# Kernel optimization log

Measured on AMD Instinct MI355X. Metric: run time of the kernel, lower is better.

Reference implementation:

```python
import jax, jax.numpy as jnp
import numpy as np

N, K, E = 100000, 256, 3200000
IN_C, H1, H2 = 5, 16, 32


def _glorot(key, shape):
    fan = shape[0]
    return jax.random.normal(key, shape, jnp.float32) / np.float32(np.sqrt(fan))


def setup_inputs() -> dict:
    key = jax.random.key(0)
    ks = jax.random.split(key, 14)
    x = jax.random.normal(ks[0], (N, IN_C), jnp.float32)
    edge_index = jax.random.randint(ks[1], (2, E), 0, N, dtype=jnp.int64)
    edge_attr = jax.random.uniform(ks[2], (E,), jnp.float32)
    pos = jax.random.uniform(ks[3], (N, K), jnp.float32)  # soft cluster assignment s_c
    return {
        "x": x, "edge_index": edge_index, "edge_attr": edge_attr, "pos": pos,
        # SplineConv1 (kernel_size=1 -> single kernel weight + root + bias)
        "W1": _glorot(ks[4], (IN_C, H1)), "root1": _glorot(ks[5], (IN_C, H1)),
        "b1": jnp.zeros((H1,), jnp.float32),
        # SplineConv2
        "W2": _glorot(ks[6], (H1, H2)), "root2": _glorot(ks[7], (H1, H2)),
        "b2": jnp.zeros((H2,), jnp.float32),
        # MLP head
        "lw1": _glorot(ks[8], (H2, 8)), "lb1": jnp.zeros((8,), jnp.float32),
        "lw2": _glorot(ks[9], (8, 2)), "lb2": jnp.zeros((2,), jnp.float32),
    }


def _leaky(v):
    return jnp.where(v > 0, v, 0.1 * v)


def reference(x, edge_index, edge_attr, pos, W1, root1, b1, W2, root2, b2, lw1, lb1, lw2, lb2):
    n = x.shape[0]
    src, dst = edge_index[0], edge_index[1]  # source_to_target flow

    # --- SplineConv(5,16,dim=1,kernel_size=1): mean_j (x_j @ W) + x @ root + b ---
    msg = x[src] @ W1                                      # [E,16]
    agg = jax.ops.segment_sum(msg, dst, num_segments=n)    # [N,16]
    deg = jax.ops.segment_sum(jnp.ones((msg.shape[0],), x.dtype), dst, num_segments=n)
    h = agg / jnp.maximum(deg, 1.0)[:, None] + x @ root1 + b1
    h = _leaky(jax.nn.relu(h))                             # relu then LeakyReLU(0.1)

    # --- pooling: x' = s_c^T h ; adj = s_c^T A s_c (A sparse with edge_attr values) ---
    xp = pos.T @ h                                          # [K,16]
    A_sc = jax.ops.segment_sum(edge_attr[:, None] * pos[dst], src, num_segments=n)  # spmm: [N,K]
    adj = pos.T @ A_sc                                      # [K,K]

    # --- nonzero/coalesce -> edge list of adj; SplineConv(16,32) on pooled graph ---
    # kernel_size=1 => edge values irrelevant; only the nonzero pattern (connectivity) matters.
    mask = (adj != 0).astype(x.dtype)                       # [K,K], row=src, col=dst
    xw = xp @ W2                                            # [K,32]
    deg2 = mask.sum(axis=0)                                 # in-degree per target
    agg2 = (mask.T @ xw) / jnp.maximum(deg2, 1.0)[:, None]
    h2 = agg2 + xp @ root2 + b2
    h2 = _leaky(jax.nn.relu(h2))                            # [K,32]

    # --- global mean pool (single graph) + MLP head, return x[0] ---
    g = h2.mean(axis=0)                                     # [32]
    out = _leaky(g @ lw1 + lb1) @ lw2 + lb2                 # [2]
    return out
```

## Files before the change

### kernel.cpp

```cpp
#include <hip/hip_runtime.h>

#define INC 5
#define H1C 16
#define H2C 32
#define KCL 256

#define NBINS 40
#define BINSZ 2500
#define MAXCHUNK 12

#define PB_SHIFT 9
#define PB_SZ 512
#define PB_NBMAX 256
#define PB_C 18432
#define PB_M 6144
#define PB_ETPB 6
#define PB_S 2
#define PB_GMAX 9216
#define PB_GETG 9

#define POOL_NB 768
#define PCH 256

typedef __attribute__((address_space(1))) const unsigned gls_src;
typedef __attribute__((address_space(3))) unsigned gls_dst;

__global__ void k_setup(const float* __restrict__ x, float* __restrict__ x8,
                        const unsigned int* __restrict__ ei, int* __restrict__ flag,
                        unsigned* __restrict__ gcur, int N, int NB) {
    int n = blockIdx.x * blockDim.x + threadIdx.x;
    if (n < N) {
        const float* xr = x + (size_t)n * INC;
        float4* o = (float4*)(x8 + (size_t)n * 8);
        o[0] = make_float4(xr[0], xr[1], xr[2], xr[3]);
        o[1] = make_float4(xr[4], 0.0f, 0.0f, 0.0f);
    }
    if (blockIdx.x == 0) {
        if (threadIdx.x < (unsigned)NB) gcur[threadIdx.x] = (unsigned)threadIdx.x * PB_C;
        if (threadIdx.x == 0) {
            int is64 = 1;
            for (int i = 1; i < 32; i += 2)
                if (ei[i] != 0u) is64 = 0;
            *flag = is64;
        }
    }
}

__global__ void k_detect(const unsigned int* __restrict__ ei, int* __restrict__ flag) {
    if (blockIdx.x == 0 && threadIdx.x == 0) {
        int is64 = 1;
        for (int i = 1; i < 32; i += 2)
            if (ei[i] != 0u) is64 = 0;
        *flag = is64;
    }
}

__global__ __launch_bounds__(1024) void k_part(const unsigned int* __restrict__ ei,
                                               const int* __restrict__ flag,
                                               unsigned* __restrict__ gcur,
                                               unsigned* __restrict__ bucket,
                                               int E, int NB) {
    __shared__ int hist[PB_NBMAX];
    __shared__ int lbase[PB_NBMAX];
    __shared__ unsigned gbase[PB_NBMAX];
    __shared__ unsigned sorted[PB_M];
    __shared__ unsigned char sbin[PB_M];

    const int tid = threadIdx.x;
    const int e0 = blockIdx.x * PB_M;
    int m = E - e0; if (m > PB_M) m = PB_M;

    for (int i = tid; i < PB_NBMAX; i += 1024) hist[i] = 0;
    __syncthreads();

    const int is64 = *flag;
    unsigned ee[PB_ETPB]; int eb[PB_ETPB]; int er[PB_ETPB];

#pragma unroll
    for (int ii = 0; ii < PB_ETPB; ii++) {
        const int off = tid + ii * 1024;
        eb[ii] = -1; ee[ii] = 0u; er[ii] = 0;
        if (off < m) {
            const int e = e0 + off;
            unsigned d, s;
            if (is64) { d = ei[2 * ((size_t)E + (size_t)e)]; s = ei[2 * (size_t)e]; }
            else      { d = ei[(size_t)E + (size_t)e];       s = ei[(size_t)e]; }
            const int b = (int)(d >> PB_SHIFT);
            eb[ii] = b;
            ee[ii] = (s << PB_SHIFT) | (d & (PB_SZ - 1));
            er[ii] = atomicAdd(&hist[b], 1);
        }
    }
    __syncthreads();

    if (tid < 64) {
        const int base = tid * 4;
        int vals[4]; int s = 0;
#pragma unroll
        for (int k = 0; k < 4; k++) { vals[k] = hist[base + k]; s += vals[k]; }
        int t = s;
#pragma unroll
        for (int off = 1; off < 64; off <<= 1) {
            int y = __shfl_up(t, off);
            if (tid >= off) t += y;
        }
        int ex = t - s;
#pragma unroll
        for (int k = 0; k < 4; k++) { lbase[base + k] = ex; ex += vals[k]; }
    }
    if (tid >= 64 && tid < 64 + NB) {
        const int b = tid - 64;
        gbase[b] = atomicAdd(&gcur[b], (unsigned)hist[b]);
    }
    __syncthreads();

#pragma unroll
    for (int ii = 0; ii < PB_ETPB; ii++) {
        if (eb[ii] >= 0) {
            const int j = lbase[eb[ii]] + er[ii];
            sorted[j] = ee[ii];
            sbin[j] = (unsigned char)eb[ii];
        }
    }
    __syncthreads();

    for (int j = tid; j < m; j += 1024) {
        const int b = (int)sbin[j];
        const unsigned g = gbase[b] + (unsigned)(j - lbase[b]);
        if (g < (unsigned)(b + 1) * PB_C) bucket[g] = sorted[j];
    }
}

__global__ __launch_bounds__(1024) void k_gather(const unsigned* __restrict__ bucket,
                                                 const unsigned* __restrict__ gcur,
                                                 const float* __restrict__ x8,
                                                 float* __restrict__ part,
                                                 int N, int NB) {
    __shared__ unsigned sorted[PB_GMAX];
    __shared__ int hist[PB_SZ];
    __shared__ int lbase[PB_SZ];
    __shared__ float stage[PB_SZ * 6];

    const int b = blockIdx.x / PB_S;
    const int sub = blockIdx.x % PB_S;
    const int tid = threadIdx.x;
    const int lo = b << PB_SHIFT;
    int hi = lo + PB_SZ; if (hi > N) hi = N;
    const int nloc = hi - lo;

    int cnt = (int)(gcur[b] - (unsigned)b * PB_C);
    if (cnt > PB_C) cnt = PB_C;
    const int i0 = (cnt * sub) / PB_S;
    const int i1 = (cnt * (sub + 1)) / PB_S;
    const int m = i1 - i0;
    const unsigned* bk = bucket + (size_t)b * PB_C + i0;

    for (int i = tid; i < PB_SZ; i += 1024) hist[i] = 0;
    __syncthreads();

    unsigned ee[PB_GETG]; int edl[PB_GETG]; int er[PB_GETG];
#pragma unroll
    for (int ii = 0; ii < PB_GETG; ii++) {
        const int off = tid + ii * 1024;
        edl[ii] = -1; ee[ii] = 0u; er[ii] = 0;
        if (off < m) {
            const unsigned e = bk[off];
            const int dl = (int)(e & (PB_SZ - 1));
            edl[ii] = dl;
            ee[ii] = e;
            er[ii] = atomicAdd(&hist[dl], 1);
        }
    }
    __syncthreads();

    if (tid < 64) {
        const int base = tid * 8;
        int vals[8]; int s = 0;
#pragma unroll
        for (int k = 0; k < 8; k++) { vals[k] = hist[base + k]; s += vals[k]; }
        int t = s;
#pragma unroll
        for (int off = 1; off < 64; off <<= 1) {
            int y = __shfl_up(t, off);
            if (tid >= off) t += y;
        }
        int ex = t - s;
#pragma unroll
        for (int k = 0; k < 8; k++) { lbase[base + k] = ex; ex += vals[k]; }
    }
    __syncthreads();

#pragma unroll
    for (int ii = 0; ii < PB_GETG; ii++)
        if (edl[ii] >= 0) sorted[lbase[edl[ii]] + er[ii]] = ee[ii];
    __syncthreads();

    const int node = tid & (PB_SZ - 1);
    const int half = tid >> PB_SHIFT;
    const int start = lbase[node];
    const int len = hist[node];
    const int js = start + (half ? (len >> 1) : 0);
    const int je = start + (half ? len : (len >> 1));
    float a0 = 0.f, a1 = 0.f, a2 = 0.f, a3 = 0.f, a4 = 0.f;
    for (int j = js; j < je; j++) {
        const unsigned s = sorted[j] >> PB_SHIFT;
        const float4 xr4 = *(const float4*)(x8 + (size_t)s * 8);
        const float xr5 = x8[(size_t)s * 8 + 4];
        a0 += xr4.x; a1 += xr4.y; a2 += xr4.z; a3 += xr4.w; a4 += xr5;
    }
    if (half) {
        float* st = stage + node * 6;
        st[0] = a0; st[1] = a1; st[2] = a2; st[3] = a3; st[4] = a4;
    }
    __syncthreads();
    if (!half && node < nloc) {
        const float* st = stage + node * 6;
        float* o = part + (size_t)sub * ((size_t)N * 6) + (size_t)(lo + node) * 6;
        o[0] = a0 + st[0];
        o[1] = a1 + st[1];
        o[2] = a2 + st[2];
        o[3] = a3 + st[3];
        o[4] = a4 + st[4];
        o[5] = (float)len;
    }
}

__global__ __launch_bounds__(1024) void k_edge_bin(const unsigned int* __restrict__ ei,
                                                   const float* __restrict__ x,
                                                   const int* __restrict__ flag,
                                                   float* __restrict__ part,
                                                   int E, int nchunk, int N) {
    __shared__ float acc[BINSZ * 6];
    const int bin = blockIdx.x % NBINS;
    const int chunk = blockIdx.x / NBINS;
    const int lo = bin * BINSZ;
    const int hi = (lo + BINSZ < N) ? (lo + BINSZ) : N;
    const int nloc = hi - lo;
    for (int i = threadIdx.x; i < nloc * 6; i += 1024) acc[i] = 0.0f;
    __syncthreads();

    const int is64 = *flag;
    const long long ce = ((long long)E + nchunk - 1) / nchunk;
    const long long e0 = (long long)chunk * ce;
    long long e1 = e0 + ce;
    if (e1 > E) e1 = E;

    for (long long e = e0 + threadIdx.x; e < e1; e += 1024) {
        const int d = is64 ? (int)ei[2 * ((size_t)E + (size_t)e)] : (int)ei[(size_t)E + (size_t)e];
        if (d >= lo && d < hi) {
            const int s = is64 ? (int)ei[2 * (size_t)e] : (int)ei[(size_t)e];
            const float* xr = x + (size_t)s * INC;
            float* a = acc + (d - lo) * 6;
            atomicAdd(a + 0, xr[0]);
            atomicAdd(a + 1, xr[1]);
            atomicAdd(a + 2, xr[2]);
            atomicAdd(a + 3, xr[3]);
            atomicAdd(a + 4, xr[4]);
            atomicAdd(a + 5, 1.0f);
        }
    }
    __syncthreads();
    float* o = part + (size_t)chunk * ((size_t)N * 6) + (size_t)lo * 6;
    for (int i = threadIdx.x; i < nloc * 6; i += 1024) o[i] = acc[i];
}

__global__ void k_node2(const float* __restrict__ x, const float* __restrict__ part,
                        const float* __restrict__ W1, const float* __restrict__ root1,
                        const float* __restrict__ b1, float* __restrict__ h,
                        int N, int nchunk) {
    int n = blockIdx.x * blockDim.x + threadIdx.x;
    if (n >= N) return;
    float s[6] = {0.f, 0.f, 0.f, 0.f, 0.f, 0.f};
    for (int c = 0; c < nchunk; c++) {
        const float* p = part + (size_t)c * ((size_t)N * 6) + (size_t)n * 6;
#pragma unroll
        for (int j = 0; j < 6; j++) s[j] += p[j];
    }
    const float inv = 1.0f / fmaxf(s[5], 1.0f);
    float xs[INC], xv[INC];
#pragma unroll
    for (int c = 0; c < INC; c++) {
        xs[c] = s[c] * inv;
        xv[c] = x[(size_t)n * INC + c];
    }
    float hv[H1C];
#pragma unroll
    for (int j = 0; j < H1C; j++) {
        float v = b1[j];
#pragma unroll
        for (int c = 0; c < INC; c++)
            v = fmaf(xs[c], W1[c * H1C + j], fmaf(xv[c], root1[c * H1C + j], v));
        hv[j] = fmaxf(v, 0.0f);
    }
    float4* hp = (float4*)(h + (size_t)n * H1C);
#pragma unroll
    for (int q = 0; q < 4; q++)
        hp[q] = make_float4(hv[4 * q], hv[4 * q + 1], hv[4 * q + 2], hv[4 * q + 3]);
}

__global__ __launch_bounds__(256) void k_pool(const float* __restrict__ pos,
                                              const float* __restrict__ h,
                                              const float* __restrict__ part,
                                              const float* __restrict__ x8,
                                              const float* __restrict__ W1,
                                              const float* __restrict__ root1,
                                              const float* __restrict__ b1,
                                              float* __restrict__ xp_part, int N, int nb) {
    __shared__ float hbuf[PCH * H1C];
    __shared__ float sred[2][32][64];
    const int tid = threadIdx.x;
    const int lane = tid & 63;
    const int w = tid >> 6;
    const int chunk = (N + nb - 1) / nb;
    const int n0 = blockIdx.x * chunk;
    const int n1 = min(n0 + chunk, N);
    const int cnt = (n1 > n0) ? (n1 - n0) : 0;

    if (part) {
        if (tid < cnt) {
            const int n = n0 + tid;
            const float* pa = part + (size_t)n * 6;
            const float* pb = part + (size_t)N * 6 + (size_t)n * 6;
            float s[6];
#pragma unroll
            for (int j = 0; j < 6; j++) s[j] = pa[j] + pb[j];
            const float inv = 1.0f / fmaxf(s[5], 1.0f);
            float xs[INC], xv[INC];
#pragma unroll
            for (int c = 0; c < INC; c++) {
                xs[c] = s[c] * inv;
                xv[c] = x8[(size_t)n * 8 + c];
            }
#pragma unroll
            for (int j = 0; j < H1C; j++) {
                float v = b1[j];
#pragma unroll
                for (int c = 0; c < INC; c++)
                    v = fmaf(xs[c], W1[c * H1C + j], fmaf(xv[c], root1[c * H1C + j], v));
                hbuf[tid * H1C + j] = fmaxf(v, 0.0f);
            }
        }
    } else {
        const size_t maxh = (size_t)N * H1C - 4;
        for (int ii = w; ii * 256 < cnt * H1C; ii += 4) {
            size_t fi = (size_t)n0 * H1C + (size_t)ii * 256 + (size_t)lane * 4;
            if (fi > maxh) fi = maxh;
            __builtin_amdgcn_global_load_lds((gls_src*)(h + fi),
                                             (gls_dst*)&hbuf[ii * 256], 16, 0, 0);
        }
    }
    __syncthreads();

    float acc[4][H1C];
#pragma unroll
    for (int c = 0; c < 4; c++)
#pragma unroll
        for (int d = 0; d < H1C; d++) acc[c][d] = 0.0f;

    const float4* pos4 = (const float4*)pos;
    const float4 z4 = make_float4(0.f, 0.f, 0.f, 0.f);

#define LDP(dst, i)                                                        \
    {                                                                      \
        const int _i = (i);                                                \
        if (_i < cnt) dst = pos4[((size_t)n0 + _i) * 64 + lane];           \
    }
#define CMP(i, p)                                                          \
    {                                                                      \
        const int _i = (i);                                                \
        if (_i < cnt) {                                                    \
            const float4 h0 = *(const float4*)&hbuf[_i * H1C + 0];         \
            const float4 h1 = *(const float4*)&hbuf[_i * H1C + 4];         \
            const float4 h2 = *(const float4*)&hbuf[_i * H1C + 8];         \
            const float4 h3 = *(const float4*)&hbuf[_i * H1C + 12];        \
            const float pk[4] = {p.x, p.y, p.z, p.w};                      \
            const float hv[H1C] = {h0.x, h0.y, h0.z, h0.w,                 \
                                   h1.x, h1.y, h1.z, h1.w,                 \
                                   h2.x, h2.y, h2.z, h2.w,                 \
                                   h3.x, h3.y, h3.z, h3.w};                \
            _Pragma("unroll")                                              \
            for (int c = 0; c < 4; c++)                                    \
                _Pragma("unroll")                                          \
                for (int d = 0; d < H1C; d++)                              \
                    acc[c][d] = fmaf(pk[c], hv[d], acc[c][d]);             \
        }                                                                  \
    }

    float4 A0 = z4, A1 = z4, A2 = z4, A3 = z4;
    float4 B0 = z4, B1 = z4, B2 = z4, B3 = z4;
    float4 C0 = z4, C1 = z4, C2 = z4, C3 = z4;
    float4 D0 = z4, D1 = z4, D2 = z4, D3 = z4;
    LDP(A0, w + 0)  LDP(A1, w + 4)  LDP(A2, w + 8)  LDP(A3, w + 12)
    LDP(B0, w + 16) LDP(B1, w + 20) LDP(B2, w + 24) LDP(B3, w + 28)
    LDP(C0, w + 32) LDP(C1, w + 36) LDP(C2, w + 40) LDP(C3, w + 44)
    LDP(D0, w + 48) LDP(D1, w + 52) LDP(D2, w + 56) LDP(D3, w + 60)
    for (int i = w; i < cnt; i += 64) {
        CMP(i + 0, A0)  CMP(i + 4, A1)  CMP(i + 8, A2)  CMP(i + 12, A3)
        LDP(A0, i + 64) LDP(A1, i + 68) LDP(A2, i + 72) LDP(A3, i + 76)
        CMP(i + 16, B0) CMP(i + 20, B1) CMP(i + 24, B2) CMP(i + 28, B3)
        LDP(B0, i + 80) LDP(B1, i + 84) LDP(B2, i + 88) LDP(B3, i + 92)
        CMP(i + 32, C0) CMP(i + 36, C1) CMP(i + 40, C2) CMP(i + 44, C3)
        LDP(C0, i + 96) LDP(C1, i + 100) LDP(C2, i + 104) LDP(C3, i + 108)
        CMP(i + 48, D0) CMP(i + 52, D1) CMP(i + 56, D2) CMP(i + 60, D3)
        LDP(D0, i + 112) LDP(D1, i + 116) LDP(D2, i + 120) LDP(D3, i + 124)
    }
#undef LDP
#undef CMP

    __syncthreads();
#pragma unroll
    for (int ch = 0; ch < 2; ch++) {
        if (w == 1 || w == 3) {
            float* sl = &sred[(w - 1) >> 1][0][0] + lane;
#pragma unroll
            for (int v = 0; v < 32; v++) sl[v * 64] = acc[ch * 2 + (v >> 4)][v & 15];
        }
        __syncthreads();
        if (w == 0 || w == 2) {
            const float* sl = &sred[w >> 1][0][0] + lane;
#pragma unroll
            for (int v = 0; v < 32; v++) acc[ch * 2 + (v >> 4)][v & 15] += sl[v * 64];
        }
        __syncthreads();
        if (w == 2) {
            float* sl = &sred[0][0][0] + lane;
#pragma unroll
            for (int v = 0; v < 32; v++) sl[v * 64] = acc[ch * 2 + (v >> 4)][v & 15];
        }
        __syncthreads();
        if (w == 0) {
            const float* sl = &sred[0][0][0] + lane;
#pragma unroll
            for (int v = 0; v < 32; v++) acc[ch * 2 + (v >> 4)][v & 15] += sl[v * 64];
        }
        __syncthreads();
    }
    if (w == 0) {
        float* o = xp_part + (size_t)blockIdx.x * (KCL * H1C);
#pragma unroll
        for (int c = 0; c < 4; c++) {
            float* oc = o + (4 * lane + c) * H1C;
            *(float4*)(oc + 0)  = make_float4(acc[c][0],  acc[c][1],  acc[c][2],  acc[c][3]);
            *(float4*)(oc + 4)  = make_float4(acc[c][4],  acc[c][5],  acc[c][6],  acc[c][7]);
            *(float4*)(oc + 8)  = make_float4(acc[c][8],  acc[c][9],  acc[c][10], acc[c][11]);
            *(float4*)(oc + 12) = make_float4(acc[c][12], acc[c][13], acc[c][14], acc[c][15]);
        }
    }
}

__global__ __launch_bounds__(1024) void k_xpred(const float* __restrict__ xp_part,
                                                float* __restrict__ xp, int nb) {
    __shared__ float r[1024];
    const int li = threadIdx.x & 63;
    const int sub = threadIdx.x >> 6;
    const int i = blockIdx.x * 64 + li;
    float s = 0.0f;
    for (int b = sub; b < nb; b += 16) s += xp_part[(size_t)b * (KCL * H1C) + i];
    r[threadIdx.x] = s;
    __syncthreads();
    if (threadIdx.x < 512) r[threadIdx.x] += r[threadIdx.x + 512];
    __syncthreads();
    if (threadIdx.x < 256) r[threadIdx.x] += r[threadIdx.x + 256];
    __syncthreads();
    if (threadIdx.x < 128) r[threadIdx.x] += r[threadIdx.x + 128];
    __syncthreads();
    if (threadIdx.x < 64) xp[i] = r[threadIdx.x] + r[threadIdx.x + 64];
}

__global__ __launch_bounds__(256) void k_tail(const float* __restrict__ xp,
                                              const float* __restrict__ W2,
                                              const float* __restrict__ root2,
                                              const float* __restrict__ b2,
                                              const float* __restrict__ lw1,
                                              const float* __restrict__ lb1,
                                              const float* __restrict__ lw2,
                                              const float* __restrict__ lb2,
                                              float* __restrict__ out) {
    __shared__ float red[4][H2C];
    __shared__ float bcast[H2C];
    const int t = threadIdx.x;
    const int wv = t >> 6;
    const int lane = t & 63;

    float row[H1C];
#pragma unroll
    for (int c = 0; c < H1C; c++) row[c] = xp[t * H1C + c];

    float v1[H2C];
#pragma unroll
    for (int j = 0; j < H2C; j++) {
        float v = 0.0f;
#pragma unroll
        for (int c = 0; c < H1C; c++) v = fmaf(row[c], W2[c * H2C + j], v);
        v1[j] = v;
    }
#pragma unroll
    for (int off = 1; off < 64; off <<= 1) {
#pragma unroll
        for (int j = 0; j < H2C; j++) v1[j] += __shfl_xor(v1[j], off);
    }
    if (lane == 0) {
#pragma unroll
        for (int j = 0; j < H2C; j++) red[wv][j] = v1[j];
    }
    __syncthreads();
    if (t < H2C) bcast[t] = red[0][t] + red[1][t] + red[2][t] + red[3][t];
    __syncthreads();

    float v2[H2C];
#pragma unroll
    for (int j = 0; j < H2C; j++) {
        float v = bcast[j] * (1.0f / KCL) + b2[j];
#pragma unroll
        for (int c = 0; c < H1C; c++) v = fmaf(row[c], root2[c * H2C + j], v);
        v2[j] = fmaxf(v, 0.0f);
    }
#pragma unroll
    for (int off = 1; off < 64; off <<= 1) {
#pragma unroll
        for (int j = 0; j < H2C; j++) v2[j] += __shfl_xor(v2[j], off);
    }
    if (lane == 0) {
#pragma unroll
        for (int j = 0; j < H2C; j++) red[wv][j] = v2[j];
    }
    __syncthreads();

    if (t == 0) {
        float g[H2C];
#pragma unroll
        for (int j = 0; j < H2C; j++)
            g[j] = (red[0][j] + red[1][j] + red[2][j] + red[3][j]) * (1.0f / KCL);
        float u[8];
#pragma unroll
        for (int a = 0; a < 8; a++) {
            float v = lb1[a];
#pragma unroll
            for (int j = 0; j < H2C; j++) v = fmaf(g[j], lw1[j * 8 + a], v);
            u[a] = v > 0.0f ? v : 0.1f * v;
        }
#pragma unroll
        for (int o = 0; o < 2; o++) {
            float v = lb2[o];
#pragma unroll
            for (int a = 0; a < 8; a++) v = fmaf(u[a], lw2[a * 2 + o], v);
            out[o] = v;
        }
    }
}

extern "C" void kernel_launch(void* const* d_in, const int* in_sizes, int n_in,
                              void* d_out, int out_size, void* d_ws, size_t ws_size,
                              hipStream_t stream) {
    const float* x         = (const float*)d_in[0];
    const unsigned int* ei = (const unsigned int*)d_in[1];
    const float* pos   = (const float*)d_in[3];
    const float* W1    = (const float*)d_in[4];
    const float* root1 = (const float*)d_in[5];
    const float* b1    = (const float*)d_in[6];
    const float* W2    = (const float*)d_in[7];
    const float* root2 = (const float*)d_in[8];
    const float* b2    = (const float*)d_in[9];
    const float* lw1   = (const float*)d_in[10];
    const float* lb1   = (const float*)d_in[11];
    const float* lw2   = (const float*)d_in[12];
    const float* lb2   = (const float*)d_in[13];
    float* out = (float*)d_out;

    const int N = in_sizes[0] / INC;
    const int E = in_sizes[1] / 2;
    const int NB = (N + PB_SZ - 1) >> PB_SHIFT;

    float* ws    = (float*)d_ws;
    float* xp    = ws;
    int*   flag  = (int*)(xp + KCL * H1C);
    float* h     = (float*)(flag + 16);
    float* regio = h + (size_t)N * H1C;

    const size_t pref_floats = (size_t)(KCL * H1C) + 16 + (size_t)N * H1C;
    const size_t region_floats = ws_size / 4 > pref_floats ? ws_size / 4 - pref_floats : 0;
    const size_t slab_floats = (size_t)POOL_NB * (KCL * H1C);
    const size_t buck_floats = (size_t)NB * PB_C + 256;
    const size_t fast_floats = (size_t)PB_S * N * 6 + (size_t)N * 8 +
                               (buck_floats > slab_floats ? buck_floats : slab_floats);

    if (region_floats >= fast_floats && N <= 131072 && NB <= PB_NBMAX) {
        float* part      = regio;
        float* x8        = part + (size_t)PB_S * N * 6;
        unsigned* bucket = (unsigned*)(x8 + (size_t)N * 8);
        unsigned* gcur   = bucket + (size_t)NB * PB_C;
        const int P = (E + PB_M - 1) / PB_M;

        k_setup<<<(N + 255) / 256, 256, 0, stream>>>(x, x8, ei, flag, gcur, N, NB);
        k_part<<<P, 1024, 0, stream>>>(ei, flag, gcur, bucket, E, NB);
        k_gather<<<NB * PB_S, 1024, 0, stream>>>(bucket, gcur, x8, part, N, NB);

        float* xp_part = (float*)bucket;
        k_pool<<<POOL_NB, 256, 0, stream>>>(pos, nullptr, part, x8, W1, root1, b1,
                                            xp_part, N, POOL_NB);
        k_xpred<<<64, 1024, 0, stream>>>(xp_part, xp, POOL_NB);
    } else {
        size_t avail = region_floats > slab_floats ? region_floats - slab_floats : 0;
        int nchunk = (int)(avail / ((size_t)N * 6));
        if (nchunk > MAXCHUNK) nchunk = MAXCHUNK;
        if (nchunk < 1) nchunk = 1;
        float* part = regio;
        float* xp_part = part + (size_t)nchunk * N * 6;
        k_detect<<<1, 64, 0, stream>>>(ei, flag);
        k_edge_bin<<<NBINS * nchunk, 1024, 0, stream>>>(ei, x, flag, part, E, nchunk, N);
        k_node2<<<(N + 255) / 256, 256, 0, stream>>>(x, part, W1, root1, b1, h, N, nchunk);
        k_pool<<<POOL_NB, 256, 0, stream>>>(pos, h, nullptr, nullptr, W1, root1, b1,
                                            xp_part, N, POOL_NB);
        k_xpred<<<64, 1024, 0, stream>>>(xp_part, xp, POOL_NB);
    }
    k_tail<<<1, 256, 0, stream>>>(xp, W2, root2, b2, lw1, lb1, lw2, lb2, out);
}
```

Baseline: 108.8 us.

## Fuse setup/partition/gather and xp-reduce/tail into cooperative grid-synced kernels

Replaces the setup, partition and gather launches with one cooperative kernel that uses grid-wide syncs between phases and grid-strides over the work items. It also merges the xp slab reduction and the tail MLP into a second cooperative kernel. The aim is to remove kernel launch gaps and dependency bubbles between the small stages. In exchange, work is squeezed into a fixed 256-block grid with grid barriers, which may reduce occupancy and latency hiding in the partition and gather phases.

```diff
diff --git a/kernel.cpp b/kernel.cpp
--- a/kernel.cpp
+++ b/kernel.cpp
@@ -1,4 +1,7 @@
 #include <hip/hip_runtime.h>
+#include <hip/hip_cooperative_groups.h>
+
+namespace cg = cooperative_groups;
 
 #define INC 5
 #define H1C 16
@@ -22,8 +25,311 @@
 #define POOL_NB 768
 #define PCH 256
 
+#define MEGA_NB 256
+
 typedef __attribute__((address_space(1))) const unsigned gls_src;
 typedef __attribute__((address_space(3))) unsigned gls_dst;
+
+struct PartL {
+    unsigned sorted[PB_M];
+    unsigned char sbin[PB_M];
+    int hist[PB_NBMAX];
+    int lbase[PB_NBMAX];
+    unsigned gbase[PB_NBMAX];
+};
+struct GathL {
+    unsigned sorted[PB_GMAX];
+    int hist[PB_SZ];
+    int lbase[PB_SZ];
+    float stage[PB_SZ * 6];
+};
+union MegaL { PartL p; GathL g; };
+
+__global__ __launch_bounds__(1024) void k_mega1(const float* __restrict__ x,
+                                                const unsigned* __restrict__ ei,
+                                                unsigned* __restrict__ gcur,
+                                                unsigned* __restrict__ bucket,
+                                                float* __restrict__ x8,
+                                                float* __restrict__ part,
+                                                int N, int E, int NB, int P) {
+    __shared__ MegaL L;
+    cg::grid_group gg = cg::this_grid();
+    const int tid = threadIdx.x;
+
+    int is64 = 1;
+#pragma unroll
+    for (int i = 1; i < 32; i += 2)
+        if (ei[i] != 0u) is64 = 0;
+
+    {
+        const int n = blockIdx.x * 1024 + tid;
+        if (n < N) {
+            const float* xr = x + (size_t)n * INC;
+            float4* o = (float4*)(x8 + (size_t)n * 8);
+            o[0] = make_float4(xr[0], xr[1], xr[2], xr[3]);
+            o[1] = make_float4(xr[4], 0.0f, 0.0f, 0.0f);
+        }
+        if (n < NB) gcur[n] = (unsigned)n * PB_C;
+    }
+    gg.sync();
+
+    for (int vb = blockIdx.x; vb < P; vb += gridDim.x) {
+        const int e0 = vb * PB_M;
+        int m = E - e0; if (m > PB_M) m = PB_M;
+
+        for (int i = tid; i < PB_NBMAX; i += 1024) L.p.hist[i] = 0;
+        __syncthreads();
+
+        unsigned ee[PB_ETPB]; int eb[PB_ETPB]; int er[PB_ETPB];
+#pragma unroll
+        for (int ii = 0; ii < PB_ETPB; ii++) {
+            const int off = tid + ii * 1024;
+            eb[ii] = -1; ee[ii] = 0u; er[ii] = 0;
+            if (off < m) {
+                const int e = e0 + off;
+                unsigned d, s;
+                if (is64) { d = ei[2 * ((size_t)E + (size_t)e)]; s = ei[2 * (size_t)e]; }
+                else      { d = ei[(size_t)E + (size_t)e];       s = ei[(size_t)e]; }
+                const int b = (int)(d >> PB_SHIFT);
+                eb[ii] = b;
+                ee[ii] = (s << PB_SHIFT) | (d & (PB_SZ - 1));
+                er[ii] = atomicAdd(&L.p.hist[b], 1);
+            }
+        }
+        __syncthreads();
+
+        if (tid < 64) {
+            const int base = tid * 4;
+            int vals[4]; int s = 0;
+#pragma unroll
+            for (int k = 0; k < 4; k++) { vals[k] = L.p.hist[base + k]; s += vals[k]; }
+            int t = s;
+#pragma unroll
+            for (int off = 1; off < 64; off <<= 1) {
+                int y = __shfl_up(t, off);
+                if (tid >= off) t += y;
+            }
+            int ex = t - s;
+#pragma unroll
+            for (int k = 0; k < 4; k++) { L.p.lbase[base + k] = ex; ex += vals[k]; }
+        }
+        if (tid >= 64 && tid < 64 + NB) {
+            const int b = tid - 64;
+            L.p.gbase[b] = atomicAdd(&gcur[b], (unsigned)L.p.hist[b]);
+        }
+        __syncthreads();
+
+#pragma unroll
+        for (int ii = 0; ii < PB_ETPB; ii++) {
+            if (eb[ii] >= 0) {
+                const int j = L.p.lbase[eb[ii]] + er[ii];
+                L.p.sorted[j] = ee[ii];
+                L.p.sbin[j] = (unsigned char)eb[ii];
+            }
+        }
+        __syncthreads();
+
+        for (int j = tid; j < m; j += 1024) {
+            const int b = (int)L.p.sbin[j];
+            const unsigned g = L.p.gbase[b] + (unsigned)(j - L.p.lbase[b]);
+            if (g < (unsigned)(b + 1) * PB_C) bucket[g] = L.p.sorted[j];
+        }
+        __syncthreads();
+    }
+    gg.sync();
+
+    for (int vb = blockIdx.x; vb < NB * PB_S; vb += gridDim.x) {
+        const int b = vb / PB_S;
+        const int sub = vb % PB_S;
+        const int lo = b << PB_SHIFT;
+        int hi = lo + PB_SZ; if (hi > N) hi = N;
+        const int nloc = hi - lo;
+
+        int cnt = (int)(gcur[b] - (unsigned)b * PB_C);
+        if (cnt > PB_C) cnt = PB_C;
+        const int i0 = (cnt * sub) / PB_S;
+        const int i1 = (cnt * (sub + 1)) / PB_S;
+        const int m = i1 - i0;
+        const unsigned* bk = bucket + (size_t)b * PB_C + i0;
+
+        for (int i = tid; i < PB_SZ; i += 1024) L.g.hist[i] = 0;
+        __syncthreads();
+
+        unsigned ee[PB_GETG]; int edl[PB_GETG]; int er[PB_GETG];
+#pragma unroll
+        for (int ii = 0; ii < PB_GETG; ii++) {
+            const int off = tid + ii * 1024;
+            edl[ii] = -1; ee[ii] = 0u; er[ii] = 0;
+            if (off < m) {
+                const unsigned e = bk[off];
+                const int dl = (int)(e & (PB_SZ - 1));
+                edl[ii] = dl;
+                ee[ii] = e;
+                er[ii] = atomicAdd(&L.g.hist[dl], 1);
+            }
+        }
+        __syncthreads();
+
+        if (tid < 64) {
+            const int base = tid * 8;
+            int vals[8]; int s = 0;
+#pragma unroll
+            for (int k = 0; k < 8; k++) { vals[k] = L.g.hist[base + k]; s += vals[k]; }
+            int t = s;
+#pragma unroll
+            for (int off = 1; off < 64; off <<= 1) {
+                int y = __shfl_up(t, off);
+                if (tid >= off) t += y;
+            }
+            int ex = t - s;
+#pragma unroll
+            for (int k = 0; k < 8; k++) { L.g.lbase[base + k] = ex; ex += vals[k]; }
+        }
+        __syncthreads();
+
+#pragma unroll
+        for (int ii = 0; ii < PB_GETG; ii++)
+            if (edl[ii] >= 0) L.g.sorted[L.g.lbase[edl[ii]] + er[ii]] = ee[ii];
+        __syncthreads();
+
+        const int node = tid & (PB_SZ - 1);
+        const int half = tid >> PB_SHIFT;
+        const int start = L.g.lbase[node];
+        const int len = L.g.hist[node];
+        const int js = start + (half ? (len >> 1) : 0);
+        const int je = start + (half ? len : (len >> 1));
+        float a0 = 0.f, a1 = 0.f, a2 = 0.f, a3 = 0.f, a4 = 0.f;
+        for (int j = js; j < je; j++) {
+            const unsigned s = L.g.sorted[j] >> PB_SHIFT;
+            const float4 xr4 = *(const float4*)(x8 + (size_t)s * 8);
+            const float xr5 = x8[(size_t)s * 8 + 4];
+            a0 += xr4.x; a1 += xr4.y; a2 += xr4.z; a3 += xr4.w; a4 += xr5;
+        }
+        if (half) {
+            float* st = L.g.stage + node * 6;
+            st[0] = a0; st[1] = a1; st[2] = a2; st[3] = a3; st[4] = a4;
+        }
+        __syncthreads();
+        if (!half && node < nloc) {
+            const float* st = L.g.stage + node * 6;
+            float* o = part + (size_t)sub * ((size_t)N * 6) + (size_t)(lo + node) * 6;
+            o[0] = a0 + st[0];
+            o[1] = a1 + st[1];
+            o[2] = a2 + st[2];
+            o[3] = a3 + st[3];
+            o[4] = a4 + st[4];
+            o[5] = (float)len;
+        }
+        __syncthreads();
+    }
+}
+
+__global__ __launch_bounds__(256) void k_mega2(const float* __restrict__ xp_part,
+                                               float* __restrict__ xp,
+                                               const float* __restrict__ W2,
+                                               const float* __restrict__ root2,
+                                               const float* __restrict__ b2,
+                                               const float* __restrict__ lw1,
+                                               const float* __restrict__ lb1,
+                                               const float* __restrict__ lw2,
+                                               const float* __restrict__ lb2,
+                                               float* __restrict__ out, int nb) {
+    cg::grid_group gg = cg::this_grid();
+    __shared__ float r[256];
+    __shared__ float red[4][H2C];
+    __shared__ float bcast[H2C];
+    const int tid = threadIdx.x;
+
+    {
+        const int li = tid & 15;
+        const int sub = tid >> 4;
+        const int i = blockIdx.x * 16 + li;
+        float s = 0.0f;
+        for (int b = sub; b < nb; b += 16) s += xp_part[(size_t)b * (KCL * H1C) + i];
+        r[tid] = s;
+        __syncthreads();
+        if (tid < 128) r[tid] += r[tid + 128];
+        __syncthreads();
+        if (tid < 64) r[tid] += r[tid + 64];
+        __syncthreads();
+        if (tid < 32) r[tid] += r[tid + 32];
+        __syncthreads();
+        if (tid < 16) xp[blockIdx.x * 16 + tid] = r[tid] + r[tid + 16];
+    }
+    gg.sync();
+
+    if (blockIdx.x == 0) {
+        const int t = tid;
+        const int wv = t >> 6;
+        const int lane = t & 63;
+
+        float row[H1C];
+#pragma unroll
+        for (int c = 0; c < H1C; c++) row[c] = xp[t * H1C + c];
+
+        float v1[H2C];
+#pragma unroll
+        for (int j = 0; j < H2C; j++) {
+            float v = 0.0f;
+#pragma unroll
+            for (int c = 0; c < H1C; c++) v = fmaf(row[c], W2[c * H2C + j], v);
+            v1[j] = v;
+        }
+#pragma unroll
+        for (int off = 1; off < 64; off <<= 1) {
+#pragma unroll
+            for (int j = 0; j < H2C; j++) v1[j] += __shfl_xor(v1[j], off);
+        }
+        if (lane == 0) {
+#pragma unroll
+            for (int j = 0; j < H2C; j++) red[wv][j] = v1[j];
+        }
+        __syncthreads();
+        if (t < H2C) bcast[t] = red[0][t] + red[1][t] + red[2][t] + red[3][t];
+        __syncthreads();
+
+        float v2[H2C];
+#pragma unroll
+        for (int j = 0; j < H2C; j++) {
+            float v = bcast[j] * (1.0f / KCL) + b2[j];
+#pragma unroll
+            for (int c = 0; c < H1C; c++) v = fmaf(row[c], root2[c * H2C + j], v);
+            v2[j] = fmaxf(v, 0.0f);
+        }
+#pragma unroll
+        for (int off = 1; off < 64; off <<= 1) {
+#pragma unroll
+            for (int j = 0; j < H2C; j++) v2[j] += __shfl_xor(v2[j], off);
+        }
+        if (lane == 0) {
+#pragma unroll
+            for (int j = 0; j < H2C; j++) red[wv][j] = v2[j];
+        }
+        __syncthreads();
+
+        if (t == 0) {
+            float g[H2C];
+#pragma unroll
+            for (int j = 0; j < H2C; j++)
+                g[j] = (red[0][j] + red[1][j] + red[2][j] + red[3][j]) * (1.0f / KCL);
+            float u[8];
+#pragma unroll
+            for (int a = 0; a < 8; a++) {
+                float v = lb1[a];
+#pragma unroll
+                for (int j = 0; j < H2C; j++) v = fmaf(g[j] , lw1[j * 8 + a], v);
+                u[a] = v > 0.0f ? v : 0.1f * v;
+            }
+#pragma unroll
+            for (int o = 0; o < 2; o++) {
+                float v = lb2[o];
+#pragma unroll
+                for (int a = 0; a < 8; a++) v = fmaf(u[a], lw2[a * 2 + o], v);
+                out[o] = v;
+            }
+        }
+    }
+}
 
 __global__ void k_setup(const float* __restrict__ x, float* __restrict__ x8,
                         const unsigned int* __restrict__ ei, int* __restrict__ flag,
@@ -567,9 +873,9 @@
     const float* lb2   = (const float*)d_in[13];
     float* out = (float*)d_out;
 
-    const int N = in_sizes[0] / INC;
-    const int E = in_sizes[1] / 2;
-    const int NB = (N + PB_SZ - 1) >> PB_SHIFT;
+    int N = in_sizes[0] / INC;
+    int E = in_sizes[1] / 2;
+    int NB = (N + PB_SZ - 1) >> PB_SHIFT;
 
     float* ws    = (float*)d_ws;
     float* xp    = ws;
@@ -584,21 +890,46 @@
     const size_t fast_floats = (size_t)PB_S * N * 6 + (size_t)N * 8 +
                                (buck_floats > slab_floats ? buck_floats : slab_floats);
 
+    int coop = 0;
+    int dev = 0;
+    hipGetDevice(&dev);
+    hipDeviceGetAttribute(&coop, hipDeviceAttributeCooperativeLaunch, dev);
+
     if (region_floats >= fast_floats && N <= 131072 && NB <= PB_NBMAX) {
         float* part      = regio;
         float* x8        = part + (size_t)PB_S * N * 6;
         unsigned* bucket = (unsigned*)(x8 + (size_t)N * 8);
         unsigned* gcur   = bucket + (size_t)NB * PB_C;
-        const int P = (E + PB_M - 1) / PB_M;
-
-        k_setup<<<(N + 255) / 256, 256, 0, stream>>>(x, x8, ei, flag, gcur, N, NB);
-        k_part<<<P, 1024, 0, stream>>>(ei, flag, gcur, bucket, E, NB);
-        k_gather<<<NB * PB_S, 1024, 0, stream>>>(bucket, gcur, x8, part, N, NB);
-
+        int P = (E + PB_M - 1) / PB_M;
         float* xp_part = (float*)bucket;
-        k_pool<<<POOL_NB, 256, 0, stream>>>(pos, nullptr, part, x8, W1, root1, b1,
-                                            xp_part, N, POOL_NB);
-        k_xpred<<<64, 1024, 0, stream>>>(xp_part, xp, POOL_NB);
+        int nb_pool = POOL_NB;
+
+        if (coop) {
+            {
+                void* a1[] = {(void*)&x, (void*)&ei, (void*)&gcur, (void*)&bucket,
+                              (void*)&x8, (void*)&part, (void*)&N, (void*)&E,
+                              (void*)&NB, (void*)&P};
+                hipLaunchCooperativeKernel((const void*)k_mega1, dim3(MEGA_NB),
+                                           dim3(1024), a1, 0, stream);
+            }
+            k_pool<<<POOL_NB, 256, 0, stream>>>(pos, nullptr, part, x8, W1, root1, b1,
+                                                xp_part, N, POOL_NB);
+            {
+                void* a2[] = {(void*)&xp_part, (void*)&xp, (void*)&W2, (void*)&root2,
+                              (void*)&b2, (void*)&lw1, (void*)&lb1, (void*)&lw2,
+                              (void*)&lb2, (void*)&out, (void*)&nb_pool};
+                hipLaunchCooperativeKernel((const void*)k_mega2, dim3(256),
+                                           dim3(256), a2, 0, stream);
+            }
+        } else {
+            k_setup<<<(N + 255) / 256, 256, 0, stream>>>(x, x8, ei, flag, gcur, N, NB);
+            k_part<<<P, 1024, 0, stream>>>(ei, flag, gcur, bucket, E, NB);
+            k_gather<<<NB * PB_S, 1024, 0, stream>>>(bucket, gcur, x8, part, N, NB);
+            k_pool<<<POOL_NB, 256, 0, stream>>>(pos, nullptr, part, x8, W1, root1, b1,
+                                                xp_part, N, POOL_NB);
+            k_xpred<<<64, 1024, 0, stream>>>(xp_part, xp, POOL_NB);
+            k_tail<<<1, 256, 0, stream>>>(xp, W2, root2, b2, lw1, lb1, lw2, lb2, out);
+        }
     } else {
         size_t avail = region_floats > slab_floats ? region_floats - slab_floats : 0;
         int nchunk = (int)(avail / ((size_t)N * 6));
@@ -612,6 +943,6 @@
         k_pool<<<POOL_NB, 256, 0, stream>>>(pos, h, nullptr, nullptr, W1, root1, b1,
                                             xp_part, N, POOL_NB);
         k_xpred<<<64, 1024, 0, stream>>>(xp_part, xp, POOL_NB);
-    }
-    k_tail<<<1, 256, 0, stream>>>(xp, W2, root2, b2, lw1, lb1, lw2, lb2, out);
-}
+        k_tail<<<1, 256, 0, stream>>>(xp, W2, root2, b2, lw1, lb1, lw2, lb2, out);
+    }
+}
```

Result: slower. 216.0 us (+98.5%).
